# Kernel optimization log

Measured on AMD Instinct MI355X. Metric: run time of the kernel, lower is better.

## Reference

```python
import jax, jax.numpy as jnp
import numpy as np

_DIR_INLIER = 0.9          # _HOUGHVOTING_DIRECTION_INLIER
_NUM_INLIER = 500          # _HOUGHVOTING_NUM_INLIER
_LABEL_THRESH = 500        # _LABEL2MASK_THRESHOL
NUM_CLASSES = 10
BS, H, W = 1, 240, 320


def setup_inputs() -> dict:
    key = jax.random.key(0)
    k_lab, k_cx, k_cy, k_nx, k_ny, k_nd = jax.random.split(key, 6)
    label = jax.random.randint(k_lab, (BS, H, W), 0, NUM_CLASSES + 1).astype(jnp.int32)
    xs = jnp.arange(W, dtype=jnp.float32)
    ys = jnp.arange(H, dtype=jnp.float32)
    xv, yv = jnp.meshgrid(xs, ys)  # [H, W] each
    # per-class ground-truth centers well inside the image so voting converges
    cxs = jax.random.uniform(k_cx, (NUM_CLASSES,), minval=40.0, maxval=W - 40.0)
    cys = jax.random.uniform(k_cy, (NUM_CLASSES,), minval=40.0, maxval=H - 40.0)
    dx = cxs[:, None, None] - xv[None]  # [C, H, W]
    dy = cys[:, None, None] - yv[None]
    nrm = jnp.sqrt(dx * dx + dy * dy) + 1e-6
    dirx = dx / nrm + 0.01 * jax.random.normal(k_nx, (NUM_CLASSES, H, W))
    diry = dy / nrm + 0.01 * jax.random.normal(k_ny, (NUM_CLASSES, H, W))
    depth = (1.0 + 0.3 * jnp.arange(NUM_CLASSES, dtype=jnp.float32))[:, None, None] \
        + 0.01 * jax.random.normal(k_nd, (NUM_CLASSES, H, W))
    cmap = jnp.stack([dirx, diry, depth], axis=1).reshape(3 * NUM_CLASSES, H, W)
    centermap = jnp.broadcast_to(cmap[None], (BS, 3 * NUM_CLASSES, H, W)).astype(jnp.float32)
    return {"label": label, "centermap": centermap}


def hough_voting(label, centermap, num_classes):
    bs, H_, W_ = label.shape
    xs = jnp.arange(W_, dtype=jnp.float32)
    ys = jnp.arange(H_, dtype=jnp.float32)
    xv, yv = jnp.meshgrid(xs, ys)            # [H, W]
    xsi = jnp.arange(W_, dtype=jnp.int32)
    all_centers, all_depths = [], []
    for b in range(bs):
        lab = label[b]
        row_c, row_d = [], []
        for cls in range(1, num_classes + 1):
            cmask = lab == cls                                    # [H, W]
            enough = cmask.sum() >= _LABEL_THRESH
            c3 = centermap[b, (cls - 1) * 3:(cls - 1) * 3 + 3]    # [3, H, W]
            slope = c3[1] / c3[0]                                  # dy/dx per pixel
            # every masked pixel votes along its line at every column x
            y_idx = jnp.round(yv[:, :, None] + slope[:, :, None] * (xs[None, None, :] - xv[:, :, None])).astype(jnp.int32)  # [H, W, W]
            valid = (y_idx >= 0) & (y_idx < H_) & cmask[:, :, None]
            bins = jnp.clip(y_idx, 0, H_ - 1) * W_ + xsi[None, None, :]
            hist = jnp.zeros(H_ * W_, jnp.float32).at[bins.ravel()].add(valid.ravel().astype(jnp.float32))
            cbin = jnp.argmax(hist)
            inlier_num = hist[cbin]
            cx = (cbin % W_).astype(jnp.float32)
            cy = (cbin // W_).astype(jnp.float32)
            # depth: mean of depth channel over direction-consistent class pixels
            disx = xv - cx
            disy = yv - cy
            dnrm = jnp.sqrt(disx * disx + disy * disy)
            dot = jnp.abs((disx / dnrm) * c3[0] + (disy / dnrm) * c3[1])  # nan at center -> compares False, as torch
            imask = (dot >= _DIR_INLIER) & cmask
            cnt = imask.sum().astype(jnp.float32)
            dsum = jnp.sum(jnp.where(imask, c3[2], 0.0))
            dmean = jnp.where(cnt > 0, dsum / jnp.maximum(cnt, 1.0), jnp.nan)
            trig = enough & (inlier_num > _NUM_INLIER)
            row_c.append(jnp.where(trig, jnp.stack([cx, cy]), jnp.zeros(2, jnp.float32)))
            row_d.append(jnp.where(trig, dmean, 0.0))
        all_centers.append(jnp.stack(row_c))
        all_depths.append(jnp.stack(row_d))
    return jnp.stack(all_centers), jnp.stack(all_depths)


def reference(label, centermap):
    return hough_voting(label, centermap, NUM_CLASSES)
```

## Files before the change

### kernel.cpp

```cpp
#include <hip/hip_runtime.h>
#include <stdint.h>

#define H 240
#define W 320
#define NPIX (H * W)
#define NCLS 10
#define COLS 4
#define BIN_BITS 20
#define BIN_MASK 0xFFFFFu


__global__ void k_init(uint32_t* ws) {
    int i = threadIdx.x;
    if (i < 128) ws[i] = 0;
}

__global__ __launch_bounds__(256) void k_compact(const int* __restrict__ label,
                                                 const float* __restrict__ cm,
                                                 uint32_t* __restrict__ cls_cnt,
                                                 uint2* __restrict__ list) {
    __shared__ uint32_t lcnt[NCLS];
    __shared__ uint32_t lbase[NCLS];
    int p = blockIdx.x * 256 + threadIdx.x;
    if (threadIdx.x < NCLS) lcnt[threadIdx.x] = 0;
    __syncthreads();

    int l = label[p];
    bool match = (l >= 1 && l <= NCLS);
    int cls = l - 1;
    uint32_t li = 0;
    if (match) li = atomicAdd(&lcnt[cls], 1u);
    __syncthreads();

    if (threadIdx.x < NCLS) {
        uint32_t c = lcnt[threadIdx.x];
        lbase[threadIdx.x] = c ? atomicAdd(&cls_cnt[threadIdx.x], c) : 0u;
    }
    __syncthreads();

    if (match) {
        float dirx = cm[(cls * 3 + 0) * NPIX + p];
        float diry = cm[(cls * 3 + 1) * NPIX + p];
        float slope = diry / dirx;
        int y = p / W, x = p - y * W;
        uint2 e;
        e.x = (uint32_t)(x | (y << 16));
        e.y = __float_as_uint(slope);
        list[cls * NPIX + lbase[cls] + li] = e;
    }
}

__global__ __launch_bounds__(256) void k_vote(const uint32_t* __restrict__ cls_cnt,
                                              const uint2* __restrict__ list,
                                              unsigned long long* __restrict__ best) {
    int cls = blockIdx.y;
    int x0 = blockIdx.x * COLS;
    __shared__ uint32_t hist[COLS][H];
    __shared__ unsigned long long wred[4];
    for (int i = threadIdx.x; i < COLS * H; i += 256) ((uint32_t*)hist)[i] = 0;
    __syncthreads();

    int n = (int)cls_cnt[cls];
    const uint2* lst = list + cls * NPIX;
    for (int i0 = 0; i0 < n; i0 += 256) {
        int i = i0 + (int)threadIdx.x;
        bool inb = (i < n);
        uint2 e;
        e.x = 0u; e.y = 0u;
        if (inb) e = lst[i];
        float slope = __uint_as_float(e.y);
        float xf = (float)(e.x & 0xFFFFu);
        float yf = (float)(e.x >> 16);
#pragma unroll
        for (int c = 0; c < COLS; ++c) {
            float dx = (float)(x0 + c) - xf;
            float r = rintf(yf + slope * dx);
            bool valid = inb && (r >= 0.0f) && (r <= (float)(H - 1));
            int bin = (int)r;
            unsigned long long vm = __ballot(valid);
            if (vm != 0ull) {
                int src = __ffsll((unsigned long long)vm) - 1;
                int b0 = __shfl(bin, src);
                unsigned long long sm = __ballot(!valid || bin == b0);
                if (sm == ~0ull) {
                    if ((int)(threadIdx.x & 63u) == src)
                        atomicAdd(&hist[c][b0], (uint32_t)__popcll(vm));
                } else if (valid) {
                    atomicAdd(&hist[c][bin], 1u);
                }
            }
        }
    }
    __syncthreads();

    unsigned long long k = 0;
    for (int i = threadIdx.x; i < COLS * H; i += 256) {
        int c = i / H, y = i - c * H;
        uint32_t v = hist[c][y];
        uint32_t bin = (uint32_t)(y * W + x0 + c);
        unsigned long long key =
            ((unsigned long long)v << BIN_BITS) | (unsigned long long)(BIN_MASK - bin);
        if (key > k) k = key;
    }
#pragma unroll
    for (int off = 32; off > 0; off >>= 1) {
        unsigned long long o = __shfl_down(k, off);
        if (o > k) k = o;
    }
    if ((threadIdx.x & 63u) == 0u) wred[threadIdx.x >> 6] = k;
    __syncthreads();
    if (threadIdx.x == 0) {
        unsigned long long kk = wred[0];
#pragma unroll
        for (int w = 1; w < 4; ++w) if (wred[w] > kk) kk = wred[w];
        atomicMax(&best[cls], kk);
    }
}

__global__ __launch_bounds__(256) void k_inlier(const int* __restrict__ label,
                                                const float* __restrict__ cm,
                                                const unsigned long long* __restrict__ best,
                                                uint32_t* __restrict__ icnt,
                                                float* __restrict__ dsum) {
    int cls = blockIdx.y;
    unsigned long long key = best[cls];
    uint32_t bin = BIN_MASK - (uint32_t)(key & BIN_MASK);
    float cx = (float)(bin % W);
    float cy = (float)(bin / W);

    const float* c0p = cm + (cls * 3 + 0) * NPIX;
    const float* c1p = cm + (cls * 3 + 1) * NPIX;
    const float* c2p = cm + (cls * 3 + 2) * NPIX;

    uint32_t lcnt = 0;
    float ldsum = 0.0f;
    int base = blockIdx.x * 2560;
    for (int i = 0; i < 10; ++i) {
        int p = base + i * 256 + threadIdx.x;
        if (label[p] == cls + 1) {
            int y = p / W, x = p - y * W;
            float disx = (float)x - cx;
            float disy = (float)y - cy;
            float dn = sqrtf(disx * disx + disy * disy);
            if (dn > 0.0f) {
                float dot = fabsf((disx / dn) * c0p[p] + (disy / dn) * c1p[p]);
                if (dot >= 0.9f) {
                    lcnt += 1;
                    ldsum += c2p[p];
                }
            }
        }
    }
#pragma unroll
    for (int off = 32; off > 0; off >>= 1) {
        ldsum += __shfl_down(ldsum, off);
        lcnt += __shfl_down(lcnt, off);
    }
    __shared__ float sd[4];
    __shared__ uint32_t sc[4];
    if ((threadIdx.x & 63u) == 0u) {
        sd[threadIdx.x >> 6] = ldsum;
        sc[threadIdx.x >> 6] = lcnt;
    }
    __syncthreads();
    if (threadIdx.x == 0) {
        float td = sd[0] + sd[1] + sd[2] + sd[3];
        uint32_t tc = sc[0] + sc[1] + sc[2] + sc[3];
        if (tc) atomicAdd(&icnt[cls], tc);
        if (td != 0.0f) atomicAdd(&dsum[cls], td);
    }
}

__global__ void k_final(const uint32_t* __restrict__ cls_cnt,
                        const unsigned long long* __restrict__ best,
                        const uint32_t* __restrict__ icnt,
                        const float* __restrict__ dsum,
                        float* __restrict__ out) {
    int cls = threadIdx.x;
    if (cls >= NCLS) return;
    unsigned long long key = best[cls];
    uint32_t hv = (uint32_t)(key >> BIN_BITS);
    uint32_t bin = BIN_MASK - (uint32_t)(key & BIN_MASK);
    float cx = (float)(bin % W);
    float cy = (float)(bin / W);
    bool trig = (cls_cnt[cls] >= 500u) && (hv > 500u);
    float c = (float)icnt[cls];
    float dm = (c > 0.0f) ? (dsum[cls] / fmaxf(c, 1.0f)) : __builtin_nanf("");
    out[cls * 2 + 0] = trig ? cx : 0.0f;
    out[cls * 2 + 1] = trig ? cy : 0.0f;
    out[2 * NCLS + cls] = trig ? dm : 0.0f;
}

extern "C" void kernel_launch(void* const* d_in, const int* in_sizes, int n_in,
                              void* d_out, int out_size, void* d_ws, size_t ws_size,
                              hipStream_t stream) {
    const int* label = (const int*)d_in[0];
    const float* cm = (const float*)d_in[1];
    float* out = (float*)d_out;
    char* ws = (char*)d_ws;

    uint32_t* cls_cnt = (uint32_t*)(ws + 0);
    unsigned long long* best = (unsigned long long*)(ws + 64);
    uint32_t* icnt = (uint32_t*)(ws + 192);
    float* dsum = (float*)(ws + 256);
    uint2* list = (uint2*)(ws + 512);

    k_init<<<1, 128, 0, stream>>>((uint32_t*)ws);
    k_compact<<<NPIX / 256, 256, 0, stream>>>(label, cm, cls_cnt, list);
    k_vote<<<dim3(W / COLS, NCLS), 256, 0, stream>>>(cls_cnt, list, best);
    k_inlier<<<dim3(30, NCLS), 256, 0, stream>>>(label, cm, best, icnt, dsum);
    k_final<<<1, 64, 0, stream>>>(cls_cnt, best, icnt, dsum, out);
}
```

Measured before the change: 114.5 us.

## Fuse inlier counting and finalization into one single-pass kernel

```diff
diff --git a/kernel.cpp b/kernel.cpp
--- a/kernel.cpp
+++ b/kernel.cpp
@@ -117,78 +117,70 @@
     }
 }
 
-__global__ __launch_bounds__(256) void k_inlier(const int* __restrict__ label,
-                                                const float* __restrict__ cm,
-                                                const unsigned long long* __restrict__ best,
-                                                uint32_t* __restrict__ icnt,
-                                                float* __restrict__ dsum) {
-    int cls = blockIdx.y;
-    unsigned long long key = best[cls];
-    uint32_t bin = BIN_MASK - (uint32_t)(key & BIN_MASK);
-    float cx = (float)(bin % W);
-    float cy = (float)(bin / W);
-
-    const float* c0p = cm + (cls * 3 + 0) * NPIX;
-    const float* c1p = cm + (cls * 3 + 1) * NPIX;
-    const float* c2p = cm + (cls * 3 + 2) * NPIX;
-
-    uint32_t lcnt = 0;
-    float ldsum = 0.0f;
-    int base = blockIdx.x * 2560;
-    for (int i = 0; i < 10; ++i) {
-        int p = base + i * 256 + threadIdx.x;
-        if (label[p] == cls + 1) {
-            int y = p / W, x = p - y * W;
-            float disx = (float)x - cx;
-            float disy = (float)y - cy;
-            float dn = sqrtf(disx * disx + disy * disy);
-            if (dn > 0.0f) {
-                float dot = fabsf((disx / dn) * c0p[p] + (disy / dn) * c1p[p]);
-                if (dot >= 0.9f) {
-                    lcnt += 1;
-                    ldsum += c2p[p];
-                }
+__global__ __launch_bounds__(256) void k_inlier_final(
+    const int* __restrict__ label, const float* __restrict__ cm,
+    const uint32_t* __restrict__ cls_cnt,
+    const unsigned long long* __restrict__ best,
+    uint32_t* __restrict__ icnt, float* __restrict__ dsum,
+    uint32_t* __restrict__ done, float* __restrict__ out) {
+    __shared__ float scx[NCLS], scy[NCLS];
+    __shared__ uint32_t scnt[NCLS];
+    __shared__ float ssum[NCLS];
+    __shared__ int slast;
+    int tid = threadIdx.x;
+    if (tid < NCLS) {
+        unsigned long long key = best[tid];
+        uint32_t bin = BIN_MASK - (uint32_t)(key & BIN_MASK);
+        scx[tid] = (float)(bin % W);
+        scy[tid] = (float)(bin / W);
+        scnt[tid] = 0u;
+        ssum[tid] = 0.0f;
+    }
+    __syncthreads();
+
+    int p = blockIdx.x * 256 + tid;
+    int l = label[p];
+    if (l >= 1 && l <= NCLS) {
+        int cls = l - 1;
+        int y = p / W, x = p - y * W;
+        float disx = (float)x - scx[cls];
+        float disy = (float)y - scy[cls];
+        float dn = sqrtf(disx * disx + disy * disy);
+        if (dn > 0.0f) {
+            float c0 = cm[(cls * 3 + 0) * NPIX + p];
+            float c1 = cm[(cls * 3 + 1) * NPIX + p];
+            float dot = fabsf((disx / dn) * c0 + (disy / dn) * c1);
+            if (dot >= 0.9f) {
+                atomicAdd(&scnt[cls], 1u);
+                atomicAdd(&ssum[cls], cm[(cls * 3 + 2) * NPIX + p]);
             }
         }
     }
-#pragma unroll
-    for (int off = 32; off > 0; off >>= 1) {
-        ldsum += __shfl_down(ldsum, off);
-        lcnt += __shfl_down(lcnt, off);
-    }
-    __shared__ float sd[4];
-    __shared__ uint32_t sc[4];
-    if ((threadIdx.x & 63u) == 0u) {
-        sd[threadIdx.x >> 6] = ldsum;
-        sc[threadIdx.x >> 6] = lcnt;
-    }
-    __syncthreads();
-    if (threadIdx.x == 0) {
-        float td = sd[0] + sd[1] + sd[2] + sd[3];
-        uint32_t tc = sc[0] + sc[1] + sc[2] + sc[3];
-        if (tc) atomicAdd(&icnt[cls], tc);
-        if (td != 0.0f) atomicAdd(&dsum[cls], td);
-    }
-}
-
-__global__ void k_final(const uint32_t* __restrict__ cls_cnt,
-                        const unsigned long long* __restrict__ best,
-                        const uint32_t* __restrict__ icnt,
-                        const float* __restrict__ dsum,
-                        float* __restrict__ out) {
-    int cls = threadIdx.x;
-    if (cls >= NCLS) return;
-    unsigned long long key = best[cls];
-    uint32_t hv = (uint32_t)(key >> BIN_BITS);
-    uint32_t bin = BIN_MASK - (uint32_t)(key & BIN_MASK);
-    float cx = (float)(bin % W);
-    float cy = (float)(bin / W);
-    bool trig = (cls_cnt[cls] >= 500u) && (hv > 500u);
-    float c = (float)icnt[cls];
-    float dm = (c > 0.0f) ? (dsum[cls] / fmaxf(c, 1.0f)) : __builtin_nanf("");
-    out[cls * 2 + 0] = trig ? cx : 0.0f;
-    out[cls * 2 + 1] = trig ? cy : 0.0f;
-    out[2 * NCLS + cls] = trig ? dm : 0.0f;
+    __syncthreads();
+
+    if (tid < NCLS) {
+        if (scnt[tid]) atomicAdd(&icnt[tid], scnt[tid]);
+        if (ssum[tid] != 0.0f) atomicAdd(&dsum[tid], ssum[tid]);
+    }
+    if (tid == 0) {
+        __threadfence();
+        uint32_t d = atomicAdd(done, 1u);
+        slast = (d == (uint32_t)(gridDim.x - 1)) ? 1 : 0;
+    }
+    __syncthreads();
+
+    if (slast && tid < NCLS) {
+        uint32_t tc = atomicAdd(&icnt[tid], 0u);
+        float td = atomicAdd(&dsum[tid], 0.0f);
+        unsigned long long key = best[tid];
+        uint32_t hv = (uint32_t)(key >> BIN_BITS);
+        bool trig = (cls_cnt[tid] >= 500u) && (hv > 500u);
+        float c = (float)tc;
+        float dm = (c > 0.0f) ? (td / fmaxf(c, 1.0f)) : __builtin_nanf("");
+        out[tid * 2 + 0] = trig ? scx[tid] : 0.0f;
+        out[tid * 2 + 1] = trig ? scy[tid] : 0.0f;
+        out[2 * NCLS + tid] = trig ? dm : 0.0f;
+    }
 }
 
 extern "C" void kernel_launch(void* const* d_in, const int* in_sizes, int n_in,
@@ -203,11 +195,12 @@
     unsigned long long* best = (unsigned long long*)(ws + 64);
     uint32_t* icnt = (uint32_t*)(ws + 192);
     float* dsum = (float*)(ws + 256);
+    uint32_t* done = (uint32_t*)(ws + 320);
     uint2* list = (uint2*)(ws + 512);
 
     k_init<<<1, 128, 0, stream>>>((uint32_t*)ws);
     k_compact<<<NPIX / 256, 256, 0, stream>>>(label, cm, cls_cnt, list);
     k_vote<<<dim3(W / COLS, NCLS), 256, 0, stream>>>(cls_cnt, list, best);
-    k_inlier<<<dim3(30, NCLS), 256, 0, stream>>>(label, cm, best, icnt, dsum);
-    k_final<<<1, 64, 0, stream>>>(cls_cnt, best, icnt, dsum, out);
-}
+    k_inlier_final<<<NPIX / 256, 256, 0, stream>>>(label, cm, cls_cnt, best,
+                                                   icnt, dsum, done, out);
+}
```

Result: faster. 107.9 us (-5.8%).
